# Performance work log

Measured on AMD Instinct MI355X. Metric: run time of the kernel, lower is better.

## Reference

```python
import jax, jax.numpy as jnp
import numpy as np

B, H, W, C = 4, 64, 64, 256
CK = C // 8  # f/g projection dim = 32


def setup_inputs() -> dict:
    key = jax.random.key(0)
    ks = jax.random.split(key, 4)
    x = jax.random.normal(ks[0], (B, H, W, C), dtype=jnp.float32)
    Wf = jax.random.normal(ks[1], (C, CK), dtype=jnp.float32) * (1.0 / np.sqrt(C))
    Wg = jax.random.normal(ks[2], (C, CK), dtype=jnp.float32) * (1.0 / np.sqrt(C))
    Wh = jax.random.normal(ks[3], (C, C), dtype=jnp.float32) * (1.0 / np.sqrt(C))
    bf = jnp.zeros((CK,), jnp.float32)
    bg = jnp.zeros((CK,), jnp.float32)
    bh = jnp.zeros((C,), jnp.float32)
    return {"x": x, "Wf": Wf, "bf": bf, "Wg": Wg, "bg": bg, "Wh": Wh, "bh": bh}


def reference(x, Wf, bf, Wg, bg, Wh, bh):
    b, h, w, c = x.shape
    n = h * w
    xf = x.reshape(b, n, c)  # 1x1 conv == per-pixel matmul
    f = xf @ Wf + bf         # [b, n, c/8]  (keys)
    g = xf @ Wg + bg         # [b, n, c/8]  (queries)
    hh = xf @ Wh + bh        # [b, n, c]    (values)
    # s[i,j] = g_i . f_j  (tf.matmul(g, f, transpose_b=True))
    s = jnp.einsum('bik,bjk->bij', g, f)
    beta = jax.nn.softmax(s, axis=-1)
    o = jnp.einsum('bij,bjc->bic', beta, hh)
    return x + o.reshape(b, h, w, c)
```

## Files before the change

kernel.cpp:

```cpp
#include <hip/hip_runtime.h>
#include <math.h>

#define CDIM 256
#define CKD  32
#define NPIX 4096
#define BATCH 4
#define NMACRO (NPIX / 64)

typedef __attribute__((ext_vector_type(8)))  short bf16x8;
typedef __attribute__((ext_vector_type(16))) float f32x16;

#if __has_builtin(__builtin_amdgcn_exp2f)
#define EXP2(x) __builtin_amdgcn_exp2f(x)
#else
#define EXP2(x) exp2f(x)
#endif

__device__ inline ushort f2bf(float x) {
    unsigned u = __float_as_uint(x);
    u += 0x7fffu + ((u >> 16) & 1u);
    return (ushort)(u >> 16);
}
__device__ inline unsigned packbf(float a, float b) {
    return (unsigned)f2bf(a) | ((unsigned)f2bf(b) << 16);
}
__device__ inline unsigned cvtpk(float a, float b) {
    unsigned r;
    asm("v_cvt_pk_bf16_f32 %0, %1, %2" : "=v"(r) : "v"(a), "v"(b));
    return r;
}
__device__ inline void lane32swap(unsigned &a, unsigned &b) {
    asm("v_permlane32_swap_b32 %0, %1" : "+v"(a), "+v"(b));
}

#define LDS_ASYNC16(gptr, lptr) \
  __builtin_amdgcn_global_load_lds((const __attribute__((address_space(1))) void*)(gptr), \
                                   (__attribute__((address_space(3))) void*)(lptr), 16, 0, 0)

__global__ __launch_bounds__(256) void prep_kernel(
    const float* __restrict__ Wh, const float* __restrict__ Wf,
    const float* __restrict__ Wg, ushort* __restrict__ Wt)
{
    __shared__ float ls[64 * 65];
    const int tid = threadIdx.x;
    const int bid = blockIdx.x;

    if (bid < 16) {
        const int k0 = (bid & 3) * 64, c0 = (bid >> 2) * 64;
        #pragma unroll
        for (int i = 0; i < 16; ++i) {
            int r = i * 4 + (tid >> 6), c = tid & 63;
            ls[r * 65 + c] = Wh[(k0 + r) * 256 + c0 + c];
        }
        __syncthreads();
        #pragma unroll
        for (int i = 0; i < 16; ++i) {
            int cr = i * 4 + (tid >> 6), k = tid & 63;
            Wt[(c0 + cr) * 256 + k0 + k] = f2bf(ls[k * 65 + cr]);
        }
    } else {
        const float* W = (bid == 16) ? Wf : Wg;
        const int rbase = 256 + (bid - 16) * 32;
        #pragma unroll
        for (int kh2 = 0; kh2 < 2; ++kh2) {
            __syncthreads();
            #pragma unroll
            for (int i = 0; i < 16; ++i) {
                int flat = i * 256 + tid;
                int k = flat >> 5, c = flat & 31;
                ls[c * 129 + k] = W[(kh2 * 128 + k) * 32 + c];
            }
            __syncthreads();
            #pragma unroll
            for (int i = 0; i < 16; ++i) {
                int flat = i * 256 + tid;
                int c = flat >> 7, k = flat & 127;
                Wt[(rbase + c) * 256 + kh2 * 128 + k] = f2bf(ls[c * 129 + k]);
            }
        }
    }
}

__global__ __launch_bounds__(256) void proj_kernel(
    const float*  __restrict__ x,
    const ushort* __restrict__ Wt,
    const float*  __restrict__ bfp, const float* __restrict__ bgp,
    const float*  __restrict__ bhp,
    ushort* __restrict__ fo,
    ushort* __restrict__ go,
    ushort* __restrict__ glo,
    ushort* __restrict__ ht)
{
    __shared__ ushort wls[2][1280 * 8];
    __shared__ ushort xls[2][128 * 8];

    const int tid  = threadIdx.x;
    const int w    = tid >> 6;
    const int lane = tid & 63;
    const int hl   = lane >> 5;
    const int ln   = lane & 31;
    const int bid  = blockIdx.x;
    const long long px0 = (long long)bid * 32;
    const int b    = (int)(px0 >> 12);
    const int n0   = (int)(px0 & (NPIX - 1));
    const int kt   = n0 >> 6;
    const int koff = n0 & 63;

    const int sx_px = tid >> 3, sx_j = tid & 7;
    const int sx_o = sx_j >> 1, sx_h = sx_j & 1;
    const int sx_slot = sx_o * 32 + ((sx_px + 2 * sx_o) & 31);

    #pragma unroll
    for (int i = 0; i < 5; ++i) {
        int s = i * 256 + tid;
        int n = s >> 2, o = ((s & 3) - (n >> 1)) & 3;
        LDS_ASYNC16(Wt + n * 256 + o * 8, &wls[0][s * 8]);
    }
    {
        float4 v = *(const float4*)(x + (px0 + sx_px) * CDIM + sx_j * 4);
        uint2 p; p.x = packbf(v.x, v.y); p.y = packbf(v.z, v.w);
        *(uint2*)&xls[0][sx_slot * 8 + sx_h * 4] = p;
    }

    f32x16 acc0={0,0,0,0,0,0,0,0,0,0,0,0,0,0,0,0};
    f32x16 acc1={0,0,0,0,0,0,0,0,0,0,0,0,0,0,0,0};
    f32x16 accfg={0,0,0,0,0,0,0,0,0,0,0,0,0,0,0,0};

    for (int sl = 0; sl < 8; ++sl) {
        const int cur = sl & 1;
        __syncthreads();
        if (sl + 1 < 8) {
            const int nxt = cur ^ 1;
            #pragma unroll
            for (int i = 0; i < 5; ++i) {
                int s = i * 256 + tid;
                int n = s >> 2, o = ((s & 3) - (n >> 1)) & 3;
                LDS_ASYNC16(Wt + n * 256 + (sl + 1) * 32 + o * 8, &wls[nxt][s * 8]);
            }
            float4 v = *(const float4*)(x + (px0 + sx_px) * CDIM + (sl + 1) * 32 + sx_j * 4);
            uint2 p; p.x = packbf(v.x, v.y); p.y = packbf(v.z, v.w);
            *(uint2*)&xls[nxt][sx_slot * 8 + sx_h * 4] = p;
        }

        #pragma unroll
        for (int st = 0; st < 2; ++st) {
            const int o = st * 2 + hl;
            #define LDW(n) (*(const bf16x8*)&wls[cur][((n) * 4 + (((o) + ((n) >> 1)) & 3)) * 8])
            bf16x8 xb  = *(const bf16x8*)&xls[cur][(o * 32 + ((ln + 2 * o) & 31)) * 8];
            bf16x8 wa0 = LDW(w * 64 + ln);
            bf16x8 wa1 = LDW(w * 64 + 32 + ln);
            acc0 = __builtin_amdgcn_mfma_f32_32x32x16_bf16(wa0, xb, acc0, 0, 0, 0);
            acc1 = __builtin_amdgcn_mfma_f32_32x32x16_bf16(wa1, xb, acc1, 0, 0, 0);
            if (w < 2) {
                bf16x8 wfg = LDW(256 + w * 32 + ln);
                accfg = __builtin_amdgcn_mfma_f32_32x32x16_bf16(xb, wfg, accfg, 0, 0, 0);
            }
            #undef LDW
        }
    }

    ushort* htt = ht + ((long long)(b * 64 + kt) * CDIM) * 64 + koff;
    #pragma unroll
    for (int r = 0; r < 16; ++r) {
        const int rowD = (r & 3) + 8 * (r >> 2) + 4 * hl;
        int c0 = w * 64 + rowD, c1 = c0 + 32;
        htt[(long long)c0 * 64 + ln] = f2bf(acc0[r] + bhp[c0]);
        htt[(long long)c1 * 64 + ln] = f2bf(acc1[r] + bhp[c1]);
    }
    if (w < 2) {
        const float bb = (w ? bgp : bfp)[ln];
        const float scl = w ? 1.44269504088896f : 1.0f;
        #pragma unroll
        for (int r = 0; r < 16; ++r) {
            const int rowD = (r & 3) + 8 * (r >> 2) + 4 * hl;
            float v = (accfg[r] + bb) * scl;
            ushort hi = f2bf(v);
            long long idx = (px0 + rowD) * CKD + ln;
            if (w == 0) {
                fo[idx] = hi;
            } else {
                go[idx] = hi;
                float hif = __uint_as_float(((unsigned)hi) << 16);
                glo[idx] = f2bf(v - hif);
            }
        }
    }
}

__global__ __launch_bounds__(256, 3) void attn_kernel(
    const float*  __restrict__ x,
    const ushort* __restrict__ fk,
    const ushort* __restrict__ gq,
    const ushort* __restrict__ glo,
    const ushort* __restrict__ hv,
    float* __restrict__ out,
    float* __restrict__ Opart,
    float* __restrict__ Lpart,
    int nks)
{
    __shared__ ushort hh_lds[2][1024 * 8];
    __shared__ ushort f_lds[2][256 * 8];
    __shared__ float  l_red[128];

    const int tid  = threadIdx.x;
    const int w    = tid >> 6;
    const int lane = tid & 63;
    const int hl   = lane >> 5;
    const int ln   = lane & 31;

    const int bid = blockIdx.x;
    const int chs = bid & 1;
    const int b   = (bid >> 1) & 3;
    const int qt  = (bid >> 3) & 31;
    const int ks  = bid >> 8;
    const int q0  = qt * 128;
    const int kt0 = (ks * NMACRO) / nks;
    const int kt1 = ((ks + 1) * NMACRO) / nks;
    const int nmac = kt1 - kt0;

    const long long bbase = (long long)b * NPIX;
    const ushort* fbase = fk + bbase * CKD;
    const ushort* htb   = hv + (long long)b * 64 * (CDIM * 64);

    const ushort* gp  = gq  + (bbase + q0 + w * 32 + ln) * CKD;
    const ushort* glp = glo + (bbase + q0 + w * 32 + ln) * CKD;
    const bf16x8 ga0 = *(const bf16x8*)(gp + hl * 8);
    const bf16x8 ga1 = *(const bf16x8*)(gp + 16 + hl * 8);
    const bf16x8 gl0 = *(const bf16x8*)(glp + hl * 8);
    const bf16x8 gl1 = *(const bf16x8*)(glp + 16 + hl * 8);

    {
        const long long tb = (long long)kt0 * (CDIM * 64);
        #pragma unroll
        for (int i = 0; i < 4; ++i) {
            int s = i * 256 + tid;
            int c = s & 127, oc = s >> 7;
            LDS_ASYNC16(htb + tb + (long long)(chs * 128 + c) * 64 + oc * 8,
                        &hh_lds[0][s * 8]);
        }
        LDS_ASYNC16(fbase + (long long)(kt0 * 64 + (tid & 63)) * CKD + (tid >> 6) * 8,
                    &f_lds[0][tid * 8]);
    }

    const f32x16 Zv = {0,0,0,0,0,0,0,0,0,0,0,0,0,0,0,0};
    f32x16 acc0={0,0,0,0,0,0,0,0,0,0,0,0,0,0,0,0};
    f32x16 acc1={0,0,0,0,0,0,0,0,0,0,0,0,0,0,0,0};
    f32x16 acc2={0,0,0,0,0,0,0,0,0,0,0,0,0,0,0,0};
    f32x16 acc3={0,0,0,0,0,0,0,0,0,0,0,0,0,0,0,0};
    float lsA = 0.f, lsB = 0.f;

    #pragma unroll 2
    for (int m = 0; m < nmac; ++m) {
        const int kt = kt0 + m;
        const int cur = m & 1;
        __syncthreads();

        if (m + 1 < nmac) {
            const int nxt = cur ^ 1;
            const long long tb = (long long)(kt + 1) * (CDIM * 64);
            #pragma unroll
            for (int i = 0; i < 4; ++i) {
                int s = i * 256 + tid;
                int c = s & 127, oc = s >> 7;
                LDS_ASYNC16(htb + tb + (long long)(chs * 128 + c) * 64 + oc * 8,
                            &hh_lds[nxt][s * 8]);
            }
            LDS_ASYNC16(fbase + (long long)((kt + 1) * 64 + (tid & 63)) * CKD + (tid >> 6) * 8,
                        &f_lds[nxt][tid * 8]);
        }

        #pragma unroll
        for (int kh = 0; kh < 2; ++kh) {
            f32x16 S, T;
            {
                bf16x8 fb0 = *(const bf16x8*)&f_lds[cur][((hl)     * 64 + kh * 32 + ln) * 8];
                bf16x8 fb1 = *(const bf16x8*)&f_lds[cur][((2 + hl) * 64 + kh * 32 + ln) * 8];
                __builtin_amdgcn_s_setprio(1);
                S = __builtin_amdgcn_mfma_f32_32x32x16_bf16(fb0, ga0, Zv, 0, 0, 0);
                T = __builtin_amdgcn_mfma_f32_32x32x16_bf16(fb0, gl0, Zv, 0, 0, 0);
                S = __builtin_amdgcn_mfma_f32_32x32x16_bf16(fb1, ga1, S, 0, 0, 0);
                T = __builtin_amdgcn_mfma_f32_32x32x16_bf16(fb1, gl1, T, 0, 0, 0);
                __builtin_amdgcn_s_setprio(0);
            }

            float p[16];
            #pragma unroll
            for (int r = 0; r < 16; ++r) {
                p[r] = EXP2(S[r] + T[r]);
                if (r & 1) lsB += p[r]; else lsA += p[r];
            }
            unsigned U[8];
            #pragma unroll
            for (int m2 = 0; m2 < 8; ++m2) U[m2] = cvtpk(p[2*m2], p[2*m2+1]);

            #pragma unroll
            for (int ck = 0; ck < 2; ++ck) {
                unsigned a0 = U[4*ck + 0], a1 = U[4*ck + 1];
                unsigned a2 = U[4*ck + 2], a3 = U[4*ck + 3];
                lane32swap(a0, a2);
                lane32swap(a1, a3);
                union { unsigned i[4]; bf16x8 v; } pf;
                pf.i[0] = a0; pf.i[1] = a1; pf.i[2] = a2; pf.i[3] = a3;
                bf16x8 pa = pf.v;
                const int oct = kh * 4 + ck * 2 + hl;
                bf16x8 hb0 = *(const bf16x8*)&hh_lds[cur][(oct * 128 +      ln) * 8];
                bf16x8 hb1 = *(const bf16x8*)&hh_lds[cur][(oct * 128 + 32 + ln) * 8];
                bf16x8 hb2 = *(const bf16x8*)&hh_lds[cur][(oct * 128 + 64 + ln) * 8];
                bf16x8 hb3 = *(const bf16x8*)&hh_lds[cur][(oct * 128 + 96 + ln) * 8];
                __builtin_amdgcn_s_setprio(1);
                acc0 = __builtin_amdgcn_mfma_f32_32x32x16_bf16(pa, hb0, acc0, 0, 0, 0);
                acc1 = __builtin_amdgcn_mfma_f32_32x32x16_bf16(pa, hb1, acc1, 0, 0, 0);
                acc2 = __builtin_amdgcn_mfma_f32_32x32x16_bf16(pa, hb2, acc2, 0, 0, 0);
                acc3 = __builtin_amdgcn_mfma_f32_32x32x16_bf16(pa, hb3, acc3, 0, 0, 0);
                __builtin_amdgcn_s_setprio(0);
            }
        }
    }

    float lsum = lsA + lsB;
    lsum += __shfl_xor(lsum, 32);
    if (hl == 0) l_red[w * 32 + ln] = lsum;
    __syncthreads();

    if (Opart) {
        const long long pb = ((long long)(ks * BATCH + b) * NPIX + q0);
        if (chs == 0 && hl == 0) Lpart[pb + w * 32 + ln] = lsum;
        #pragma unroll
        for (int r = 0; r < 16; ++r) {
            int rowD = (r & 3) + 8 * (r >> 2) + 4 * hl;
            int ql = w * 32 + rowD;
            long long rg = (pb + ql) * CDIM + chs * 128 + ln;
            Opart[rg]      = acc0[r];
            Opart[rg + 32] = acc1[r];
            Opart[rg + 64] = acc2[r];
            Opart[rg + 96] = acc3[r];
        }
    } else {
        #pragma unroll
        for (int r = 0; r < 16; ++r) {
            int rowD = (r & 3) + 8 * (r >> 2) + 4 * hl;
            int ql = w * 32 + rowD;
            float linv = 1.f / l_red[ql];
            long long rg = (bbase + q0 + ql) * CDIM + chs * 128 + ln;
            out[rg]      = x[rg]      + acc0[r] * linv;
            out[rg + 32] = x[rg + 32] + acc1[r] * linv;
            out[rg + 64] = x[rg + 64] + acc2[r] * linv;
            out[rg + 96] = x[rg + 96] + acc3[r] * linv;
        }
    }
}

__global__ __launch_bounds__(256) void combine_kernel(
    const float* __restrict__ x, const float* __restrict__ Op,
    const float* __restrict__ Lp, float* __restrict__ out, int nks)
{
    const int tid = threadIdx.x, w = tid >> 6, lane = tid & 63;
    const int row = blockIdx.x * 4 + w;
    const int b = row >> 12, q = row & (NPIX - 1);

    float l = 0.f;
    for (int ks = 0; ks < nks; ++ks)
        l += Lp[(ks * BATCH + b) * NPIX + q];
    const float linv = 1.f / l;

    float4 a = {0.f, 0.f, 0.f, 0.f};
    for (int ks = 0; ks < nks; ++ks) {
        const float4 v = *(const float4*)&Op[
            (((long long)(ks * BATCH + b) * NPIX + q)) * CDIM + lane * 4];
        a.x += v.x; a.y += v.y; a.z += v.z; a.w += v.w;
    }
    const long long g = ((long long)b * NPIX + q) * CDIM + lane * 4;
    const float4 xv = *(const float4*)&x[g];
    float4 o;
    o.x = xv.x + a.x * linv;
    o.y = xv.y + a.y * linv;
    o.z = xv.z + a.z * linv;
    o.w = xv.w + a.w * linv;
    *(float4*)&out[g] = o;
}

extern "C" void kernel_launch(void* const* d_in, const int* in_sizes, int n_in,
                              void* d_out, int out_size, void* d_ws, size_t ws_size,
                              hipStream_t stream) {
    const float* x  = (const float*)d_in[0];
    const float* Wf = (const float*)d_in[1];
    const float* bf = (const float*)d_in[2];
    const float* Wg = (const float*)d_in[3];
    const float* bg = (const float*)d_in[4];
    const float* Wh = (const float*)d_in[5];
    const float* bh = (const float*)d_in[6];
    float* out = (float*)d_out;

    ushort* fbf = (ushort*)d_ws;
    ushort* gbf = fbf + BATCH * NPIX * CKD;
    ushort* glo = gbf + BATCH * NPIX * CKD;
    ushort* ht  = glo + BATCH * NPIX * CKD;
    ushort* Wt  = ht + BATCH * NPIX * CDIM;
    char*   pb  = (char*)(Wt + 320 * 256);

    const int NKS = 3;
    const size_t base_used = (size_t)(pb - (char*)d_ws);
    const size_t oelems = (size_t)NKS * BATCH * NPIX * CDIM;
    const size_t lelems = (size_t)NKS * BATCH * NPIX;
    float* Opart = nullptr;
    float* Lpart = nullptr;
    int nks = 1;
    if (ws_size >= base_used + (oelems + lelems) * sizeof(float)) {
        nks = NKS;
        Opart = (float*)pb;
        Lpart = Opart + oelems;
    }

    prep_kernel<<<dim3(18), 256, 0, stream>>>(Wh, Wf, Wg, Wt);
    proj_kernel<<<dim3(512), 256, 0, stream>>>(x, Wt, bf, bg, bh, fbf, gbf, glo, ht);
    attn_kernel<<<dim3(256 * nks), 256, 0, stream>>>(x, fbf, gbf, glo, ht, out,
                                                     Opart, Lpart, nks);
    if (nks > 1)
        combine_kernel<<<dim3(BATCH * NPIX / 4), 256, 0, stream>>>(x, Opart, Lpart, out, nks);
}
```

Measured before the change: 161.8 us.

## Load K and V tiles directly from global memory instead of staging through LDS

Removes the double-buffered LDS staging of the f (keys) and hh (values) tiles along with the per-iteration __syncthreads, and has each wave read its MFMA operands straight from global memory (relying on L1/L2). This drops barrier and LDS traffic and frees LDS, which could allow more occupancy. In exchange each of the four waves separately fetches the same K/V data from cache, there is no explicit prefetch overlap, and the global loads are 16-byte accesses strided by row that may coalesce poorly.

After: 235.9 us. +45.7%, slower.

```diff
diff --git a/kernel.cpp b/kernel.cpp
--- a/kernel.cpp
+++ b/kernel.cpp
@@ -198,9 +198,7 @@
     float* __restrict__ Lpart,
     int nks)
 {
-    __shared__ ushort hh_lds[2][1024 * 8];
-    __shared__ ushort f_lds[2][256 * 8];
-    __shared__ float  l_red[128];
+    __shared__ float l_red[128];
 
     const int tid  = threadIdx.x;
     const int w    = tid >> 6;
@@ -216,11 +214,12 @@
     const int q0  = qt * 128;
     const int kt0 = (ks * NMACRO) / nks;
     const int kt1 = ((ks + 1) * NMACRO) / nks;
-    const int nmac = kt1 - kt0;
 
     const long long bbase = (long long)b * NPIX;
     const ushort* fbase = fk + bbase * CKD;
     const ushort* htb   = hv + (long long)b * 64 * (CDIM * 64);
+    const ushort* fpl = fbase + (long long)(hl * 8);
+    const ushort* hpl = htb + (long long)(chs * 128 + ln) * 64;
 
     const ushort* gp  = gq  + (bbase + q0 + w * 32 + ln) * CKD;
     const ushort* glp = glo + (bbase + q0 + w * 32 + ln) * CKD;
@@ -229,19 +228,6 @@
     const bf16x8 gl0 = *(const bf16x8*)(glp + hl * 8);
     const bf16x8 gl1 = *(const bf16x8*)(glp + 16 + hl * 8);
 
-    {
-        const long long tb = (long long)kt0 * (CDIM * 64);
-        #pragma unroll
-        for (int i = 0; i < 4; ++i) {
-            int s = i * 256 + tid;
-            int c = s & 127, oc = s >> 7;
-            LDS_ASYNC16(htb + tb + (long long)(chs * 128 + c) * 64 + oc * 8,
-                        &hh_lds[0][s * 8]);
-        }
-        LDS_ASYNC16(fbase + (long long)(kt0 * 64 + (tid & 63)) * CKD + (tid >> 6) * 8,
-                    &f_lds[0][tid * 8]);
-    }
-
     const f32x16 Zv = {0,0,0,0,0,0,0,0,0,0,0,0,0,0,0,0};
     f32x16 acc0={0,0,0,0,0,0,0,0,0,0,0,0,0,0,0,0};
     f32x16 acc1={0,0,0,0,0,0,0,0,0,0,0,0,0,0,0,0};
@@ -250,38 +236,22 @@
     float lsA = 0.f, lsB = 0.f;
 
     #pragma unroll 2
-    for (int m = 0; m < nmac; ++m) {
-        const int kt = kt0 + m;
-        const int cur = m & 1;
-        __syncthreads();
-
-        if (m + 1 < nmac) {
-            const int nxt = cur ^ 1;
-            const long long tb = (long long)(kt + 1) * (CDIM * 64);
-            #pragma unroll
-            for (int i = 0; i < 4; ++i) {
-                int s = i * 256 + tid;
-                int c = s & 127, oc = s >> 7;
-                LDS_ASYNC16(htb + tb + (long long)(chs * 128 + c) * 64 + oc * 8,
-                            &hh_lds[nxt][s * 8]);
-            }
-            LDS_ASYNC16(fbase + (long long)((kt + 1) * 64 + (tid & 63)) * CKD + (tid >> 6) * 8,
-                        &f_lds[nxt][tid * 8]);
-        }
+    for (int kt = kt0; kt < kt1; ++kt) {
+        const ushort* hmac = hpl + (long long)kt * 16384;
 
         #pragma unroll
         for (int kh = 0; kh < 2; ++kh) {
+            const ushort* fK = fpl + (long long)(kt * 64 + kh * 32 + ln) * CKD;
+            bf16x8 fb0 = *(const bf16x8*)(fK);
+            bf16x8 fb1 = *(const bf16x8*)(fK + 16);
+
             f32x16 S, T;
-            {
-                bf16x8 fb0 = *(const bf16x8*)&f_lds[cur][((hl)     * 64 + kh * 32 + ln) * 8];
-                bf16x8 fb1 = *(const bf16x8*)&f_lds[cur][((2 + hl) * 64 + kh * 32 + ln) * 8];
-                __builtin_amdgcn_s_setprio(1);
-                S = __builtin_amdgcn_mfma_f32_32x32x16_bf16(fb0, ga0, Zv, 0, 0, 0);
-                T = __builtin_amdgcn_mfma_f32_32x32x16_bf16(fb0, gl0, Zv, 0, 0, 0);
-                S = __builtin_amdgcn_mfma_f32_32x32x16_bf16(fb1, ga1, S, 0, 0, 0);
-                T = __builtin_amdgcn_mfma_f32_32x32x16_bf16(fb1, gl1, T, 0, 0, 0);
-                __builtin_amdgcn_s_setprio(0);
-            }
+            __builtin_amdgcn_s_setprio(1);
+            S = __builtin_amdgcn_mfma_f32_32x32x16_bf16(fb0, ga0, Zv, 0, 0, 0);
+            T = __builtin_amdgcn_mfma_f32_32x32x16_bf16(fb0, gl0, Zv, 0, 0, 0);
+            S = __builtin_amdgcn_mfma_f32_32x32x16_bf16(fb1, ga1, S, 0, 0, 0);
+            T = __builtin_amdgcn_mfma_f32_32x32x16_bf16(fb1, gl1, T, 0, 0, 0);
+            __builtin_amdgcn_s_setprio(0);
 
             float p[16];
             #pragma unroll
@@ -293,6 +263,7 @@
             #pragma unroll
             for (int m2 = 0; m2 < 8; ++m2) U[m2] = cvtpk(p[2*m2], p[2*m2+1]);
 
+            const ushort* hK = hmac + (kh * 4 + hl) * 8;
             #pragma unroll
             for (int ck = 0; ck < 2; ++ck) {
                 unsigned a0 = U[4*ck + 0], a1 = U[4*ck + 1];
@@ -302,11 +273,10 @@
                 union { unsigned i[4]; bf16x8 v; } pf;
                 pf.i[0] = a0; pf.i[1] = a1; pf.i[2] = a2; pf.i[3] = a3;
                 bf16x8 pa = pf.v;
-                const int oct = kh * 4 + ck * 2 + hl;
-                bf16x8 hb0 = *(const bf16x8*)&hh_lds[cur][(oct * 128 +      ln) * 8];
-                bf16x8 hb1 = *(const bf16x8*)&hh_lds[cur][(oct * 128 + 32 + ln) * 8];
-                bf16x8 hb2 = *(const bf16x8*)&hh_lds[cur][(oct * 128 + 64 + ln) * 8];
-                bf16x8 hb3 = *(const bf16x8*)&hh_lds[cur][(oct * 128 + 96 + ln) * 8];
+                bf16x8 hb0 = *(const bf16x8*)(hK + ck * 16);
+                bf16x8 hb1 = *(const bf16x8*)(hK + ck * 16 + 2048);
+                bf16x8 hb2 = *(const bf16x8*)(hK + ck * 16 + 4096);
+                bf16x8 hb3 = *(const bf16x8*)(hK + ck * 16 + 6144);
                 __builtin_amdgcn_s_setprio(1);
                 acc0 = __builtin_amdgcn_mfma_f32_32x32x16_bf16(pa, hb0, acc0, 0, 0, 0);
                 acc1 = __builtin_amdgcn_mfma_f32_32x32x16_bf16(pa, hb1, acc1, 0, 0, 0);
```
